# Kernel tuning notes

Hardware: AMD Instinct MI355X
Metric: run time of the kernel (lower is better)

The kernel has to match this reference:

```python
import jax, jax.numpy as jnp
import numpy as np

N0, N1, N2 = 120000, 40000, 10000   # sampled node counts per hop
E0, E1 = 600000, 150000             # edges per block (fanout ~15)
DIN, DH, NC = 128, 256, 47


def _glorot(k, fan_in, fan_out):
    s = (2.0 / (fan_in + fan_out)) ** 0.5
    return jax.random.normal(k, (fan_in, fan_out), jnp.float32) * s


def setup_inputs() -> dict:
    key = jax.random.key(0)
    ks = jax.random.split(key, 20)
    x0 = jax.random.normal(ks[0], (N0, DIN), jnp.float32)
    src0 = jax.random.randint(ks[1], (E0,), 0, N0)
    dst0 = jax.random.randint(ks[2], (E0,), 0, N1)
    src1 = jax.random.randint(ks[3], (E1,), 0, N1)
    dst1 = jax.random.randint(ks[4], (E1,), 0, N2)
    srcb0 = jax.random.randint(ks[5], (E0,), 0, N0)
    dstb0 = jax.random.randint(ks[6], (E0,), 0, N1)
    srcb1 = jax.random.randint(ks[7], (E1,), 0, N1)
    dstb1 = jax.random.randint(ks[8], (E1,), 0, N2)
    # id_old_value_new: must satisfy idx[:n] < n for every truncation length n,
    # i.e. idx[k] in [0, k+1)
    rng = np.random.default_rng(0)
    idx = jnp.asarray((rng.random(N0) * (np.arange(N0) + 1)).astype(np.int64))
    mix_ratio = jnp.float32(0.5)
    Wl0 = _glorot(ks[9], DIN, DH); Wr0 = _glorot(ks[10], DIN, DH)
    b0 = jnp.zeros((DH,), jnp.float32)
    Wl1 = _glorot(ks[11], DH, DH); Wr1 = _glorot(ks[12], DH, DH)
    b1 = jnp.zeros((DH,), jnp.float32)
    Wlin = _glorot(ks[13], DH, NC)
    blin = jnp.zeros((NC,), jnp.float32)
    return dict(x0=x0, src0=src0, dst0=dst0, src1=src1, dst1=dst1,
                srcb0=srcb0, dstb0=dstb0, srcb1=srcb1, dstb1=dstb1,
                idx=idx, mix_ratio=mix_ratio,
                Wl0=Wl0, Wr0=Wr0, b0=b0, Wl1=Wl1, Wr1=Wr1, b1=b1,
                Wlin=Wlin, blin=blin)


def _sage(x_all, root_x, src, dst, n_root, Wl, Wr, b):
    # PyG-style SAGEConv, mean aggregation: lin_l(mean_j x_j) + lin_r(root)
    msgs = x_all[src]                                        # [E, D] gather
    s = jax.ops.segment_sum(msgs, dst, num_segments=n_root)  # [n_root, D]
    cnt = jax.ops.segment_sum(jnp.ones_like(dst, dtype=x_all.dtype), dst,
                              num_segments=n_root)
    mean = s / jnp.maximum(cnt, 1.0)[:, None]
    return mean @ Wl + root_x @ Wr + b


def reference(x0, src0, dst0, src1, dst1, srcb0, dstb0, srcb1, dstb1,
              idx, mix_ratio, Wl0, Wr0, b0, Wl1, Wr1, b1, Wlin, blin):
    blocks = [(src0, dst0, N1), (src1, dst1, N2)]
    blocks_b = [(srcb0, dstb0, N1), (srcb1, dstb1, N2)]
    params = [(Wl0, Wr0, b0), (Wl1, Wr1, b1)]
    m = mix_ratio

    # first branch (dropout omitted: inference mode)
    aggr_xs = [x0]
    for i in range(2):
        src, dst, n_root = blocks[i]
        Wl, Wr, b = params[i]
        root_x = aggr_xs[-1][:n_root]
        x = jax.nn.relu(_sage(aggr_xs[-1], root_x, src, dst, n_root, Wl, Wr, b))
        aggr_xs.append(x)

    # permuted branch via id_old_value_new gather
    aggr_xs_b = [x[idx[: x.shape[0]]] for x in aggr_xs]

    x_mix = aggr_xs[0] * m + aggr_xs_b[0] * (1.0 - m)
    for i in range(2):
        src, dst, n_root = blocks[i]
        srcb, dstb, n_root_b = blocks_b[i]
        Wl, Wr, b = params[i]
        x_new = jax.nn.relu(_sage(aggr_xs[i], x_mix[:n_root], src, dst,
                                  n_root, Wl, Wr, b))
        x_new_b = jax.nn.relu(_sage(aggr_xs_b[i], x_mix[:n_root_b], srcb, dstb,
                                    n_root_b, Wl, Wr, b))
        x_mix = x_new * m + x_new_b * (1.0 - m)

    logits = x_mix @ Wlin + blin
    return jax.nn.log_softmax(logits, axis=-1)
```

## Files before the change

kernel.cpp:

```cpp
#include <hip/hip_runtime.h>
#include <math.h>

#define N1C 40000
#define N2C 10000
#define DIN 128
#define DH  256
#define NC  47

#define TOTCNT (2 * N1C + 2 * N2C)
#define CAP 64

typedef __attribute__((ext_vector_type(8))) short v8s;
typedef __attribute__((ext_vector_type(4))) float v4f;

__device__ __forceinline__ unsigned short f2bf(float f) {
    unsigned int u = __float_as_uint(f);
    u += 0x7FFF + ((u >> 16) & 1);
    return (unsigned short)(u >> 16);
}
__device__ __forceinline__ float bf2f(unsigned int h) {
    return __uint_as_float(h << 16);
}

__device__ __forceinline__ unsigned char f2e4m3(float f) {
    unsigned int u = __float_as_uint(f);
    unsigned char s = (unsigned char)((u >> 24) & 0x80);
    float a = __uint_as_float(u & 0x7FFFFFFF);
    if (a > 448.0f) a = 448.0f;
    if (a < 0.015625f) {
        int k = (int)rintf(a * 512.0f);
        return s | (unsigned char)k;
    }
    unsigned int bits = __float_as_uint(a);
    int et = (int)(bits >> 23) - 127 + 7;
    unsigned int m32 = bits & 0x7FFFFF;
    unsigned int m3 = m32 >> 20;
    unsigned int rest = m32 & 0xFFFFF;
    if (rest > 0x80000 || (rest == 0x80000 && (m3 & 1))) m3++;
    if (m3 == 8) { m3 = 0; et++; }
    if (et > 15 || (et == 15 && m3 == 7)) return s | 0x7E;
    return s | (unsigned char)((et << 3) | m3);
}

__device__ __forceinline__ void build_lut(float* lut, int t) {
    if (t < 256) {
        int e = (t >> 3) & 15, mm = t & 7;
        float d = (e == 0) ? (float)mm * (1.0f / 512.0f)
                           : (1.0f + (float)mm * 0.125f) * exp2f((float)(e - 7));
        if (t & 0x80) d = -d;
        lut[t] = d;
    }
}

__global__ __launch_bounds__(256) void front_fused(
        const int* __restrict__ src0, const int* __restrict__ dst0,
        const int* __restrict__ srcb0, const int* __restrict__ dstb0,
        const int* __restrict__ src1, const int* __restrict__ dst1,
        const int* __restrict__ srcb1, const int* __restrict__ dstb1,
        const int* __restrict__ perm, int* __restrict__ cur,
        int* __restrict__ bucket, int E0, int E1, int nbFill,
        const float* __restrict__ x0, unsigned short* __restrict__ x0h,
        unsigned char* __restrict__ x0f, long n8, int nbConv,
        const float* __restrict__ Wl0, const float* __restrict__ Wr0,
        const float* __restrict__ Wl1, const float* __restrict__ Wr1,
        unsigned short* __restrict__ Wt0l, unsigned short* __restrict__ Wt0r,
        unsigned short* __restrict__ Wt1l, unsigned short* __restrict__ Wt1r) {
    int b = blockIdx.x, t = threadIdx.x;
    if (b < nbFill) {
        int e = b * 256 + t;
        int tot = 2 * E0 + 2 * E1;
        if (e >= tot) return;
        int s, bin;
        if (e < E0) {
            s = src0[e];                  bin = dst0[e];
        } else if (e < 2 * E0) {
            int le = e - E0;
            s = perm[srcb0[le]];          bin = N1C + dstb0[le];
        } else if (e < 2 * E0 + E1) {
            int le = e - 2 * E0;
            s = src1[le];                 bin = 2 * N1C + dst1[le];
        } else {
            int le = e - 2 * E0 - E1;
            s = perm[srcb1[le]];          bin = 2 * N1C + N2C + dstb1[le];
        }
        int pos = atomicAdd(&cur[bin], 1);
        if (pos < CAP) bucket[(size_t)bin * CAP + pos] = s;
    } else if (b < nbFill + nbConv) {
        long i = (long)(b - nbFill) * 256 + t;
        if (i >= n8) return;
        const float4* p = (const float4*)(x0 + i * 8);
        float4 a = p[0], c = p[1];
        float f[8] = {a.x, a.y, a.z, a.w, c.x, c.y, c.z, c.w};
        v8s o;
        unsigned int q0 = 0, q1 = 0;
#pragma unroll
        for (int j = 0; j < 8; j++) {
            o[j] = (short)f2bf(f[j]);
            unsigned int e8 = f2e4m3(f[j]);
            if (j < 4) q0 |= e8 << (8 * j); else q1 |= e8 << (8 * (j - 4));
        }
        *(v8s*)(x0h + i * 8) = o;
        uint2 q = {q0, q1};
        *(uint2*)(x0f + i * 8) = q;
    } else {
        int id = (b - nbFill - nbConv) * 256 + t;
        const int S0 = DIN * DH;
        const int S1 = DH * DH;
        const float* W; unsigned short* Wt; int K, loc;
        if (id < S0)                   { W = Wl0; Wt = Wt0l; K = DIN; loc = id; }
        else if (id < 2 * S0)          { W = Wr0; Wt = Wt0r; K = DIN; loc = id - S0; }
        else if (id < 2 * S0 + S1)     { W = Wl1; Wt = Wt1l; K = DH;  loc = id - 2 * S0; }
        else if (id < 2 * S0 + 2 * S1) { W = Wr1; Wt = Wt1r; K = DH;  loc = id - 2 * S0 - S1; }
        else return;
        int n = loc / K, k = loc - n * K;
        Wt[(size_t)n * K + k] = f2bf(W[(size_t)k * DH + n]);
    }
}

__global__ __launch_bounds__(256) void gather_mean_128f(
        const unsigned char* __restrict__ xf, const int* __restrict__ bucket,
        const int* __restrict__ cur, unsigned short* __restrict__ mean0,
        unsigned short* __restrict__ meanb0) {
    __shared__ float lut[256];
    build_lut(lut, threadIdx.x);
    __syncthreads();
    const int half = N1C / 4;
    int b = blockIdx.x;
    int binbase; unsigned short* outp; int rb;
    if (b < half) { binbase = 0;   outp = mean0;  rb = b; }
    else          { binbase = N1C; outp = meanb0; rb = b - half; }
    int row = rb * 4 + (threadIdx.x >> 6);
    int lane = threadIdx.x & 63;
    int bin = binbase + row;
    int cnt = min(cur[bin], CAP);
    const int* cs = bucket + (size_t)bin * CAP;
    float a0 = 0.0f, a1 = 0.0f;
    int i = 0;
    for (; i + 3 < cnt; i += 4) {
        int s0 = cs[i], s1 = cs[i + 1], s2 = cs[i + 2], s3 = cs[i + 3];
        unsigned int u0 = *(const unsigned short*)&xf[(size_t)s0 * DIN + lane * 2];
        unsigned int u1 = *(const unsigned short*)&xf[(size_t)s1 * DIN + lane * 2];
        unsigned int u2 = *(const unsigned short*)&xf[(size_t)s2 * DIN + lane * 2];
        unsigned int u3 = *(const unsigned short*)&xf[(size_t)s3 * DIN + lane * 2];
        a0 += lut[u0 & 0xFF] + lut[u1 & 0xFF] + lut[u2 & 0xFF] + lut[u3 & 0xFF];
        a1 += lut[u0 >> 8] + lut[u1 >> 8] + lut[u2 >> 8] + lut[u3 >> 8];
    }
    for (; i < cnt; i++) {
        unsigned int u = *(const unsigned short*)&xf[(size_t)cs[i] * DIN + lane * 2];
        a0 += lut[u & 0xFF];
        a1 += lut[u >> 8];
    }
    float inv = 1.0f / (float)max(cnt, 1);
    unsigned int o = (unsigned int)f2bf(a0 * inv) | ((unsigned int)f2bf(a1 * inv) << 16);
    *(unsigned int*)&outp[(size_t)row * DIN + lane * 2] = o;
}

__global__ __launch_bounds__(256) void gather_mean_256f(
        const unsigned char* __restrict__ xf, const int* __restrict__ bucket,
        const int* __restrict__ cur, unsigned short* __restrict__ mean1,
        unsigned short* __restrict__ meanb1) {
    __shared__ float lut[256];
    build_lut(lut, threadIdx.x);
    __syncthreads();
    const int half = N2C / 4;
    int b = blockIdx.x;
    int binbase; unsigned short* outp; int rb;
    if (b < half) { binbase = 2 * N1C;       outp = mean1;  rb = b; }
    else          { binbase = 2 * N1C + N2C; outp = meanb1; rb = b - half; }
    int row = rb * 4 + (threadIdx.x >> 6);
    int lane = threadIdx.x & 63;
    int bin = binbase + row;
    int cnt = min(cur[bin], CAP);
    const int* cs = bucket + (size_t)bin * CAP;
    float a0 = 0.0f, a1 = 0.0f, a2 = 0.0f, a3 = 0.0f;
    int i = 0;
    for (; i + 1 < cnt; i += 2) {
        unsigned int u = *(const unsigned int*)&xf[(size_t)cs[i] * DH + lane * 4];
        unsigned int v = *(const unsigned int*)&xf[(size_t)cs[i + 1] * DH + lane * 4];
        a0 += lut[u & 0xFF] + lut[v & 0xFF];
        a1 += lut[(u >> 8) & 0xFF] + lut[(v >> 8) & 0xFF];
        a2 += lut[(u >> 16) & 0xFF] + lut[(v >> 16) & 0xFF];
        a3 += lut[u >> 24] + lut[v >> 24];
    }
    if (i < cnt) {
        unsigned int u = *(const unsigned int*)&xf[(size_t)cs[i] * DH + lane * 4];
        a0 += lut[u & 0xFF]; a1 += lut[(u >> 8) & 0xFF];
        a2 += lut[(u >> 16) & 0xFF]; a3 += lut[u >> 24];
    }
    float inv = 1.0f / (float)max(cnt, 1);
    uint2 o;
    o.x = (unsigned int)f2bf(a0 * inv) | ((unsigned int)f2bf(a1 * inv) << 16);
    o.y = (unsigned int)f2bf(a2 * inv) | ((unsigned int)f2bf(a3 * inv) << 16);
    *(uint2*)&outp[(size_t)row * DH + lane * 4] = o;
}

#define KP0 136
#define H0T 5
__global__ __launch_bounds__(256, 2) void hop0_mfma(
        const unsigned short* __restrict__ x0h, const int* __restrict__ idx,
        const unsigned short* __restrict__ mean0, const unsigned short* __restrict__ meanb0,
        const unsigned short* __restrict__ Wtl, const unsigned short* __restrict__ Wtr,
        const float* __restrict__ b, const float* __restrict__ mixp,
        unsigned char* __restrict__ x1f, unsigned short* __restrict__ xm1) {
    __shared__ unsigned short Alds[4][16][KP0];
    int t = threadIdx.x;
    int wv = t >> 6, lane = t & 63;
    int mrow = lane & 15, quad = lane >> 4;
    float m = *mixp;

    v8s wl[4][4], wr[4][4];
    float bb[4];
#pragma unroll
    for (int ct = 0; ct < 4; ct++) {
        int n = wv * 64 + ct * 16 + mrow;
        bb[ct] = b[n];
#pragma unroll
        for (int ks = 0; ks < 4; ks++) {
            int k0 = ks * 32 + quad * 8;
            wl[ct][ks] = *(const v8s*)&Wtl[(size_t)n * DIN + k0];
            wr[ct][ks] = *(const v8s*)&Wtr[(size_t)n * DIN + k0];
        }
    }

    for (int tile = 0; tile < H0T; tile++) {
        int row0 = (blockIdx.x * H0T + tile) * 16;
        {
            int r = t >> 4, k0 = (t & 15) * 8;
            int rg = row0 + r;
            *(v8s*)&Alds[0][r][k0] = *(const v8s*)&mean0[(size_t)rg * DIN + k0];
            *(v8s*)&Alds[1][r][k0] = *(const v8s*)&meanb0[(size_t)rg * DIN + k0];
            v8s xr = *(const v8s*)&x0h[(size_t)rg * DIN + k0];
            int ib = idx[rg];
            v8s xb = *(const v8s*)&x0h[(size_t)ib * DIN + k0];
            v8s vm;
#pragma unroll
            for (int j = 0; j < 8; j++) {
                float fr = bf2f((unsigned short)xr[j]);
                float fb = bf2f((unsigned short)xb[j]);
                vm[j] = (short)f2bf(m * fr + (1.0f - m) * fb);
            }
            *(v8s*)&Alds[2][r][k0] = xr;
            *(v8s*)&Alds[3][r][k0] = vm;
        }
        __syncthreads();
        v4f accA[4], accB[4], accC[4], accD[4];
#pragma unroll
        for (int ct = 0; ct < 4; ct++) {
            accA[ct] = (v4f){0.f, 0.f, 0.f, 0.f}; accB[ct] = (v4f){0.f, 0.f, 0.f, 0.f};
            accC[ct] = (v4f){0.f, 0.f, 0.f, 0.f}; accD[ct] = (v4f){0.f, 0.f, 0.f, 0.f};
        }
#pragma unroll
        for (int ks = 0; ks < 4; ks++) {
            int k0 = ks * 32 + quad * 8;
            v8s aM = *(v8s*)&Alds[0][mrow][k0];
            v8s aB = *(v8s*)&Alds[1][mrow][k0];
            v8s aR = *(v8s*)&Alds[2][mrow][k0];
            v8s aX = *(v8s*)&Alds[3][mrow][k0];
#pragma unroll
            for (int ct = 0; ct < 4; ct++) {
                accA[ct] = __builtin_amdgcn_mfma_f32_16x16x32_bf16(aM, wl[ct][ks], accA[ct], 0, 0, 0);
                accB[ct] = __builtin_amdgcn_mfma_f32_16x16x32_bf16(aB, wl[ct][ks], accB[ct], 0, 0, 0);
                accC[ct] = __builtin_amdgcn_mfma_f32_16x16x32_bf16(aR, wr[ct][ks], accC[ct], 0, 0, 0);
                accD[ct] = __builtin_amdgcn_mfma_f32_16x16x32_bf16(aX, wr[ct][ks], accD[ct], 0, 0, 0);
            }
        }
#pragma unroll
        for (int ct = 0; ct < 4; ct++) {
            int col = wv * 64 + ct * 16 + mrow;
#pragma unroll
            for (int r = 0; r < 4; r++) {
                int row = row0 + quad * 4 + r;
                float pA = accA[ct][r], pB = accB[ct][r], pC = accC[ct][r], pD = accD[ct][r];
                float xv  = fmaxf(pA + pC + bb[ct], 0.0f);
                float xn  = fmaxf(pA + pD + bb[ct], 0.0f);
                float xnb = fmaxf(pB + pD + bb[ct], 0.0f);
                x1f[(size_t)row * DH + col] = f2e4m3(xv);
                xm1[(size_t)row * DH + col] = f2bf(m * xn + (1.0f - m) * xnb);
            }
        }
        __syncthreads();
    }
}

#define KP1 264
#define H1T 2
__global__ __launch_bounds__(256, 2) void hop1_mfma(
        const unsigned short* __restrict__ mean1, const unsigned short* __restrict__ meanb1,
        const unsigned short* __restrict__ xm1,
        const unsigned short* __restrict__ Wtl, const unsigned short* __restrict__ Wtr,
        const float* __restrict__ b, const float* __restrict__ mixp,
        float* __restrict__ xm2) {
    __shared__ unsigned short Alds[3][16][KP1];
    int t = threadIdx.x;
    int wv = t >> 6, lane = t & 63;
    int mrow = lane & 15, quad = lane >> 4;
    float m = *mixp;

    v8s wlc[4][4], wrc[4][4];
    float bb[4];
#pragma unroll
    for (int ct = 0; ct < 4; ct++) {
        int n = wv * 64 + ct * 16 + mrow;
        bb[ct] = b[n];
#pragma unroll
        for (int ks = 0; ks < 4; ks++) {
            int k0 = ks * 32 + quad * 8;
            wlc[ct][ks] = *(const v8s*)&Wtl[(size_t)n * DH + k0];
            wrc[ct][ks] = *(const v8s*)&Wtr[(size_t)n * DH + k0];
        }
    }

    for (int tt = 0; tt < H1T; tt++) {
        int tIdx = blockIdx.x * H1T + tt;
        if (tIdx >= N2C / 16) break;
        int row0 = tIdx * 16;
        {
            int r = t >> 4, k0 = (t & 15) * 16;
            int rg = row0 + r;
            *(v8s*)&Alds[0][r][k0]     = *(const v8s*)&mean1[(size_t)rg * DH + k0];
            *(v8s*)&Alds[0][r][k0 + 8] = *(const v8s*)&mean1[(size_t)rg * DH + k0 + 8];
            *(v8s*)&Alds[1][r][k0]     = *(const v8s*)&meanb1[(size_t)rg * DH + k0];
            *(v8s*)&Alds[1][r][k0 + 8] = *(const v8s*)&meanb1[(size_t)rg * DH + k0 + 8];
            *(v8s*)&Alds[2][r][k0]     = *(const v8s*)&xm1[(size_t)rg * DH + k0];
            *(v8s*)&Alds[2][r][k0 + 8] = *(const v8s*)&xm1[(size_t)rg * DH + k0 + 8];
        }
        __syncthreads();
        v4f accA[4], accB[4], accC[4];
#pragma unroll
        for (int ct = 0; ct < 4; ct++) {
            accA[ct] = (v4f){0.f, 0.f, 0.f, 0.f};
            accB[ct] = (v4f){0.f, 0.f, 0.f, 0.f};
            accC[ct] = (v4f){0.f, 0.f, 0.f, 0.f};
        }
#pragma unroll
        for (int ks = 0; ks < 8; ks++) {
            int k0 = ks * 32 + quad * 8;
            v8s aM = *(v8s*)&Alds[0][mrow][k0];
            v8s aB = *(v8s*)&Alds[1][mrow][k0];
            v8s aR = *(v8s*)&Alds[2][mrow][k0];
#pragma unroll
            for (int ct = 0; ct < 4; ct++) {
                v8s bl, br;
                if (ks < 4) { bl = wlc[ct][ks]; br = wrc[ct][ks]; }
                else {
                    int n = wv * 64 + ct * 16 + mrow;
                    bl = *(const v8s*)&Wtl[(size_t)n * DH + k0];
                    br = *(const v8s*)&Wtr[(size_t)n * DH + k0];
                }
                accA[ct] = __builtin_amdgcn_mfma_f32_16x16x32_bf16(aM, bl, accA[ct], 0, 0, 0);
                accB[ct] = __builtin_amdgcn_mfma_f32_16x16x32_bf16(aB, bl, accB[ct], 0, 0, 0);
                accC[ct] = __builtin_amdgcn_mfma_f32_16x16x32_bf16(aR, br, accC[ct], 0, 0, 0);
            }
        }
#pragma unroll
        for (int ct = 0; ct < 4; ct++) {
            int col = wv * 64 + ct * 16 + mrow;
#pragma unroll
            for (int r = 0; r < 4; r++) {
                int row = row0 + quad * 4 + r;
                float xn  = fmaxf(accA[ct][r] + accC[ct][r] + bb[ct], 0.0f);
                float xnb = fmaxf(accB[ct][r] + accC[ct][r] + bb[ct], 0.0f);
                xm2[(size_t)row * DH + col] = m * xn + (1.0f - m) * xnb;
            }
        }
        __syncthreads();
    }
}

__global__ __launch_bounds__(256) void logits_lsm(
        const float* __restrict__ xmix2, const float* __restrict__ Wlin,
        const float* __restrict__ blin, float* __restrict__ out, int nrows) {
    int w = threadIdx.x >> 6;
    int row = blockIdx.x * 4 + w;
    if (row >= nrows) return;
    int t = threadIdx.x & 63;
    __shared__ float xs[4][DH];
    for (int i = t; i < DH; i += 64) xs[w][i] = xmix2[(size_t)row * DH + i];
    __builtin_amdgcn_s_waitcnt(0);
    float acc = 0.0f;
    if (t < NC) {
        acc = blin[t];
        for (int k = 0; k < DH; k++) acc += xs[w][k] * Wlin[k * NC + t];
    }
    float v = (t < NC) ? acc : -INFINITY;
    float mx = v;
    for (int off = 32; off; off >>= 1) mx = fmaxf(mx, __shfl_xor(mx, off, 64));
    float ex = (t < NC) ? expf(acc - mx) : 0.0f;
    float sum = ex;
    for (int off = 32; off; off >>= 1) sum += __shfl_xor(sum, off, 64);
    if (t < NC) out[(size_t)row * NC + t] = acc - mx - logf(sum);
}

extern "C" void kernel_launch(void* const* d_in, const int* in_sizes, int n_in,
                              void* d_out, int out_size, void* d_ws, size_t ws_size,
                              hipStream_t stream) {
    const float* x0    = (const float*)d_in[0];
    const int*   src0  = (const int*)d_in[1];
    const int*   dst0  = (const int*)d_in[2];
    const int*   src1  = (const int*)d_in[3];
    const int*   dst1  = (const int*)d_in[4];
    const int*   srcb0 = (const int*)d_in[5];
    const int*   dstb0 = (const int*)d_in[6];
    const int*   srcb1 = (const int*)d_in[7];
    const int*   dstb1 = (const int*)d_in[8];
    const int*   idx   = (const int*)d_in[9];
    const float* mixp  = (const float*)d_in[10];
    const float* Wl0   = (const float*)d_in[11];
    const float* Wr0   = (const float*)d_in[12];
    const float* b0    = (const float*)d_in[13];
    const float* Wl1   = (const float*)d_in[14];
    const float* Wr1   = (const float*)d_in[15];
    const float* b1    = (const float*)d_in[16];
    const float* Wlin  = (const float*)d_in[17];
    const float* blin  = (const float*)d_in[18];
    float* out = (float*)d_out;

    const int E0 = in_sizes[1];
    const int E1 = in_sizes[3];
    const long x0elems = (long)in_sizes[0];

    int* wsi    = (int*)d_ws;
    int* cur    = wsi;
    int* bucket = cur + TOTCNT;
    unsigned short* wsh = (unsigned short*)(bucket + (size_t)TOTCNT * CAP);
    unsigned short* mean0  = wsh;
    unsigned short* meanb0 = mean0  + (size_t)N1C * DIN;
    unsigned short* mean1  = meanb0 + (size_t)N1C * DIN;
    unsigned short* meanb1 = mean1  + (size_t)N2C * DH;
    unsigned short* xm1h   = meanb1 + (size_t)N2C * DH;
    unsigned short* x0h    = xm1h   + (size_t)N1C * DH;
    unsigned short* Wt0l   = x0h    + (size_t)x0elems;
    unsigned short* Wt0r   = Wt0l + DIN * DH;
    unsigned short* Wt1l   = Wt0r + DIN * DH;
    unsigned short* Wt1r   = Wt1l + DH * DH;
    unsigned char* x0f = (unsigned char*)(Wt1r + DH * DH);
    unsigned char* x1f = x0f + (size_t)x0elems;
    float* xm2 = (float*)(x1f + (size_t)N1C * DH + 8);

    hipMemsetAsync(cur, 0, sizeof(int) * TOTCNT, stream);

    int etot = 2 * E0 + 2 * E1;
    int nbFill = (etot + 255) / 256;
    long n8 = x0elems / 8;
    int nbConv = (int)((n8 + 255) / 256);
    int nbW = (2 * DIN * DH + 2 * DH * DH + 255) / 256;
    front_fused<<<nbFill + nbConv + nbW, 256, 0, stream>>>(
        src0, dst0, srcb0, dstb0, src1, dst1, srcb1, dstb1, idx, cur, bucket,
        E0, E1, nbFill, x0, x0h, x0f, n8, nbConv,
        Wl0, Wr0, Wl1, Wr1, Wt0l, Wt0r, Wt1l, Wt1r);

    gather_mean_128f<<<2 * (N1C / 4), 256, 0, stream>>>(x0f, bucket, cur, mean0, meanb0);

    hop0_mfma<<<N1C / (16 * H0T), 256, 0, stream>>>(x0h, idx, mean0, meanb0, Wt0l, Wt0r,
                                                    b0, mixp, x1f, xm1h);

    gather_mean_256f<<<2 * (N2C / 4), 256, 0, stream>>>(x1f, bucket, cur, mean1, meanb1);

    hop1_mfma<<<(N2C / 16 + H1T - 1) / H1T, 256, 0, stream>>>(mean1, meanb1, xm1h,
                                                              Wt1l, Wt1r, b1, mixp, xm2);

    logits_lsm<<<(N2C + 3) / 4, 256, 0, stream>>>(xm2, Wlin, blin, out, N2C);
}
```

Before: 383.6 us.

## Use hardware FP8 decode, widen 128-dim gather, drop bf16 copy of x0

Replaces the shared-memory LUT FP8 decode with the packed fp8-to-f32 conversion builtin when the compiler provides it. The 128-wide gather now has each lane load 4 bytes, so one wavefront covers two rows and the block count is halved. The bf16 copy of x0 is no longer written in the front kernel; hop0 reads the fp32 x0 directly and converts to bf16 itself. This removes a full bf16 write of x0 and its later re-read, but hop0 now loads twice as many bytes for the root and permuted rows, and the hardware path depends on the builtin's FP8 format matching the software e4m3 encoding.

Result: faster. 366.3 us (-4.5%).

```diff
diff --git a/kernel.cpp b/kernel.cpp
--- a/kernel.cpp
+++ b/kernel.cpp
@@ -12,6 +12,11 @@
 
 typedef __attribute__((ext_vector_type(8))) short v8s;
 typedef __attribute__((ext_vector_type(4))) float v4f;
+typedef __attribute__((ext_vector_type(2))) float v2f;
+
+#if __has_builtin(__builtin_amdgcn_cvt_pk_f32_fp8)
+#define HW_FP8 1
+#endif
 
 __device__ __forceinline__ unsigned short f2bf(float f) {
     unsigned int u = __float_as_uint(f);
@@ -42,6 +47,7 @@
     return s | (unsigned char)((et << 3) | m3);
 }
 
+#ifndef HW_FP8
 __device__ __forceinline__ void build_lut(float* lut, int t) {
     if (t < 256) {
         int e = (t >> 3) & 15, mm = t & 7;
@@ -51,6 +57,19 @@
         lut[t] = d;
     }
 }
+#endif
+
+__device__ __forceinline__ void dec4(unsigned int u, float& f0, float& f1,
+                                     float& f2, float& f3, const float* lut) {
+#ifdef HW_FP8
+    v2f lo = __builtin_amdgcn_cvt_pk_f32_fp8((int)u, false);
+    v2f hi = __builtin_amdgcn_cvt_pk_f32_fp8((int)u, true);
+    f0 = lo[0]; f1 = lo[1]; f2 = hi[0]; f3 = hi[1];
+#else
+    f0 = lut[u & 0xFF]; f1 = lut[(u >> 8) & 0xFF];
+    f2 = lut[(u >> 16) & 0xFF]; f3 = lut[u >> 24];
+#endif
+}
 
 __global__ __launch_bounds__(256) void front_fused(
         const int* __restrict__ src0, const int* __restrict__ dst0,
@@ -59,8 +78,8 @@
         const int* __restrict__ srcb1, const int* __restrict__ dstb1,
         const int* __restrict__ perm, int* __restrict__ cur,
         int* __restrict__ bucket, int E0, int E1, int nbFill,
-        const float* __restrict__ x0, unsigned short* __restrict__ x0h,
-        unsigned char* __restrict__ x0f, long n8, int nbConv,
+        const float* __restrict__ x0, unsigned char* __restrict__ x0f,
+        long n8, int nbConv,
         const float* __restrict__ Wl0, const float* __restrict__ Wr0,
         const float* __restrict__ Wl1, const float* __restrict__ Wr1,
         unsigned short* __restrict__ Wt0l, unsigned short* __restrict__ Wt0r,
@@ -91,15 +110,12 @@
         const float4* p = (const float4*)(x0 + i * 8);
         float4 a = p[0], c = p[1];
         float f[8] = {a.x, a.y, a.z, a.w, c.x, c.y, c.z, c.w};
-        v8s o;
         unsigned int q0 = 0, q1 = 0;
 #pragma unroll
         for (int j = 0; j < 8; j++) {
-            o[j] = (short)f2bf(f[j]);
             unsigned int e8 = f2e4m3(f[j]);
             if (j < 4) q0 |= e8 << (8 * j); else q1 |= e8 << (8 * (j - 4));
         }
-        *(v8s*)(x0h + i * 8) = o;
         uint2 q = {q0, q1};
         *(uint2*)(x0f + i * 8) = q;
     } else {
@@ -121,47 +137,61 @@
         const unsigned char* __restrict__ xf, const int* __restrict__ bucket,
         const int* __restrict__ cur, unsigned short* __restrict__ mean0,
         unsigned short* __restrict__ meanb0) {
-    __shared__ float lut[256];
-    build_lut(lut, threadIdx.x);
+#ifndef HW_FP8
+    __shared__ float lutm[256];
+    build_lut(lutm, threadIdx.x);
     __syncthreads();
-    const int half = N1C / 4;
+    const float* lut = lutm;
+#else
+    const float* lut = nullptr;
+#endif
+    const int half = N1C / 8;
     int b = blockIdx.x;
     int binbase; unsigned short* outp; int rb;
     if (b < half) { binbase = 0;   outp = mean0;  rb = b; }
     else          { binbase = N1C; outp = meanb0; rb = b - half; }
-    int row = rb * 4 + (threadIdx.x >> 6);
-    int lane = threadIdx.x & 63;
+    int wv = threadIdx.x >> 6, lane = threadIdx.x & 63;
+    int row = rb * 8 + wv * 2 + (lane >> 5);
+    int c4 = (lane & 31) * 4;
     int bin = binbase + row;
     int cnt = min(cur[bin], CAP);
     const int* cs = bucket + (size_t)bin * CAP;
-    float a0 = 0.0f, a1 = 0.0f;
+    float a0 = 0.0f, a1 = 0.0f, a2 = 0.0f, a3 = 0.0f;
     int i = 0;
-    for (; i + 3 < cnt; i += 4) {
-        int s0 = cs[i], s1 = cs[i + 1], s2 = cs[i + 2], s3 = cs[i + 3];
-        unsigned int u0 = *(const unsigned short*)&xf[(size_t)s0 * DIN + lane * 2];
-        unsigned int u1 = *(const unsigned short*)&xf[(size_t)s1 * DIN + lane * 2];
-        unsigned int u2 = *(const unsigned short*)&xf[(size_t)s2 * DIN + lane * 2];
-        unsigned int u3 = *(const unsigned short*)&xf[(size_t)s3 * DIN + lane * 2];
-        a0 += lut[u0 & 0xFF] + lut[u1 & 0xFF] + lut[u2 & 0xFF] + lut[u3 & 0xFF];
-        a1 += lut[u0 >> 8] + lut[u1 >> 8] + lut[u2 >> 8] + lut[u3 >> 8];
-    }
-    for (; i < cnt; i++) {
-        unsigned int u = *(const unsigned short*)&xf[(size_t)cs[i] * DIN + lane * 2];
-        a0 += lut[u & 0xFF];
-        a1 += lut[u >> 8];
+    for (; i + 1 < cnt; i += 2) {
+        int s0 = cs[i], s1 = cs[i + 1];
+        unsigned int u = *(const unsigned int*)&xf[(size_t)s0 * DIN + c4];
+        unsigned int v = *(const unsigned int*)&xf[(size_t)s1 * DIN + c4];
+        float u0, u1, u2, u3, w0, w1, w2, w3;
+        dec4(u, u0, u1, u2, u3, lut);
+        dec4(v, w0, w1, w2, w3, lut);
+        a0 += u0 + w0; a1 += u1 + w1; a2 += u2 + w2; a3 += u3 + w3;
+    }
+    if (i < cnt) {
+        unsigned int u = *(const unsigned int*)&xf[(size_t)cs[i] * DIN + c4];
+        float u0, u1, u2, u3;
+        dec4(u, u0, u1, u2, u3, lut);
+        a0 += u0; a1 += u1; a2 += u2; a3 += u3;
     }
     float inv = 1.0f / (float)max(cnt, 1);
-    unsigned int o = (unsigned int)f2bf(a0 * inv) | ((unsigned int)f2bf(a1 * inv) << 16);
-    *(unsigned int*)&outp[(size_t)row * DIN + lane * 2] = o;
+    uint2 o;
+    o.x = (unsigned int)f2bf(a0 * inv) | ((unsigned int)f2bf(a1 * inv) << 16);
+    o.y = (unsigned int)f2bf(a2 * inv) | ((unsigned int)f2bf(a3 * inv) << 16);
+    *(uint2*)&outp[(size_t)row * DIN + c4] = o;
 }
 
 __global__ __launch_bounds__(256) void gather_mean_256f(
         const unsigned char* __restrict__ xf, const int* __restrict__ bucket,
         const int* __restrict__ cur, unsigned short* __restrict__ mean1,
         unsigned short* __restrict__ meanb1) {
-    __shared__ float lut[256];
-    build_lut(lut, threadIdx.x);
+#ifndef HW_FP8
+    __shared__ float lutm[256];
+    build_lut(lutm, threadIdx.x);
     __syncthreads();
+    const float* lut = lutm;
+#else
+    const float* lut = nullptr;
+#endif
     const int half = N2C / 4;
     int b = blockIdx.x;
     int binbase; unsigned short* outp; int rb;
@@ -175,17 +205,19 @@
     float a0 = 0.0f, a1 = 0.0f, a2 = 0.0f, a3 = 0.0f;
     int i = 0;
     for (; i + 1 < cnt; i += 2) {
-        unsigned int u = *(const unsigned int*)&xf[(size_t)cs[i] * DH + lane * 4];
-        unsigned int v = *(const unsigned int*)&xf[(size_t)cs[i + 1] * DH + lane * 4];
-        a0 += lut[u & 0xFF] + lut[v & 0xFF];
-        a1 += lut[(u >> 8) & 0xFF] + lut[(v >> 8) & 0xFF];
-        a2 += lut[(u >> 16) & 0xFF] + lut[(v >> 16) & 0xFF];
-        a3 += lut[u >> 24] + lut[v >> 24];
+        int s0 = cs[i], s1 = cs[i + 1];
+        unsigned int u = *(const unsigned int*)&xf[(size_t)s0 * DH + lane * 4];
+        unsigned int v = *(const unsigned int*)&xf[(size_t)s1 * DH + lane * 4];
+        float u0, u1, u2, u3, w0, w1, w2, w3;
+        dec4(u, u0, u1, u2, u3, lut);
+        dec4(v, w0, w1, w2, w3, lut);
+        a0 += u0 + w0; a1 += u1 + w1; a2 += u2 + w2; a3 += u3 + w3;
     }
     if (i < cnt) {
         unsigned int u = *(const unsigned int*)&xf[(size_t)cs[i] * DH + lane * 4];
-        a0 += lut[u & 0xFF]; a1 += lut[(u >> 8) & 0xFF];
-        a2 += lut[(u >> 16) & 0xFF]; a3 += lut[u >> 24];
+        float u0, u1, u2, u3;
+        dec4(u, u0, u1, u2, u3, lut);
+        a0 += u0; a1 += u1; a2 += u2; a3 += u3;
     }
     float inv = 1.0f / (float)max(cnt, 1);
     uint2 o;
@@ -197,7 +229,7 @@
 #define KP0 136
 #define H0T 5
 __global__ __launch_bounds__(256, 2) void hop0_mfma(
-        const unsigned short* __restrict__ x0h, const int* __restrict__ idx,
+        const float* __restrict__ x0, const int* __restrict__ idx,
         const unsigned short* __restrict__ mean0, const unsigned short* __restrict__ meanb0,
         const unsigned short* __restrict__ Wtl, const unsigned short* __restrict__ Wtr,
         const float* __restrict__ b, const float* __restrict__ mixp,
@@ -229,17 +261,20 @@
             int rg = row0 + r;
             *(v8s*)&Alds[0][r][k0] = *(const v8s*)&mean0[(size_t)rg * DIN + k0];
             *(v8s*)&Alds[1][r][k0] = *(const v8s*)&meanb0[(size_t)rg * DIN + k0];
-            v8s xr = *(const v8s*)&x0h[(size_t)rg * DIN + k0];
+            const float4* xr4 = (const float4*)&x0[(size_t)rg * DIN + k0];
+            float4 A0 = xr4[0], A1 = xr4[1];
             int ib = idx[rg];
-            v8s xb = *(const v8s*)&x0h[(size_t)ib * DIN + k0];
-            v8s vm;
+            const float4* xb4 = (const float4*)&x0[(size_t)ib * DIN + k0];
+            float4 B0 = xb4[0], B1 = xb4[1];
+            float fa[8] = {A0.x, A0.y, A0.z, A0.w, A1.x, A1.y, A1.z, A1.w};
+            float fb[8] = {B0.x, B0.y, B0.z, B0.w, B1.x, B1.y, B1.z, B1.w};
+            v8s vr, vm;
 #pragma unroll
             for (int j = 0; j < 8; j++) {
-                float fr = bf2f((unsigned short)xr[j]);
-                float fb = bf2f((unsigned short)xb[j]);
-                vm[j] = (short)f2bf(m * fr + (1.0f - m) * fb);
+                vr[j] = (short)f2bf(fa[j]);
+                vm[j] = (short)f2bf(m * fa[j] + (1.0f - m) * fb[j]);
             }
-            *(v8s*)&Alds[2][r][k0] = xr;
+            *(v8s*)&Alds[2][r][k0] = vr;
             *(v8s*)&Alds[3][r][k0] = vm;
         }
         __syncthreads();
@@ -428,14 +463,13 @@
     unsigned short* mean1  = meanb0 + (size_t)N1C * DIN;
     unsigned short* meanb1 = mean1  + (size_t)N2C * DH;
     unsigned short* xm1h   = meanb1 + (size_t)N2C * DH;
-    unsigned short* x0h    = xm1h   + (size_t)N1C * DH;
-    unsigned short* Wt0l   = x0h    + (size_t)x0elems;
+    unsigned short* Wt0l   = xm1h   + (size_t)N1C * DH;
     unsigned short* Wt0r   = Wt0l + DIN * DH;
     unsigned short* Wt1l   = Wt0r + DIN * DH;
     unsigned short* Wt1r   = Wt1l + DH * DH;
-    unsigned char* x0f = (unsigned char*)(Wt1r + DH * DH);
+    float* xm2 = (float*)(Wt1r + DH * DH);
+    unsigned char* x0f = (unsigned char*)(xm2 + (size_t)N2C * DH);
     unsigned char* x1f = x0f + (size_t)x0elems;
-    float* xm2 = (float*)(x1f + (size_t)N1C * DH + 8);
 
     hipMemsetAsync(cur, 0, sizeof(int) * TOTCNT, stream);
 
@@ -446,12 +480,12 @@
     int nbW = (2 * DIN * DH + 2 * DH * DH + 255) / 256;
     front_fused<<<nbFill + nbConv + nbW, 256, 0, stream>>>(
         src0, dst0, srcb0, dstb0, src1, dst1, srcb1, dstb1, idx, cur, bucket,
-        E0, E1, nbFill, x0, x0h, x0f, n8, nbConv,
+        E0, E1, nbFill, x0, x0f, n8, nbConv,
         Wl0, Wr0, Wl1, Wr1, Wt0l, Wt0r, Wt1l, Wt1r);
 
-    gather_mean_128f<<<2 * (N1C / 4), 256, 0, stream>>>(x0f, bucket, cur, mean0, meanb0);
-
-    hop0_mfma<<<N1C / (16 * H0T), 256, 0, stream>>>(x0h, idx, mean0, meanb0, Wt0l, Wt0r,
+    gather_mean_128f<<<2 * (N1C / 8), 256, 0, stream>>>(x0f, bucket, cur, mean0, meanb0);
+
+    hop0_mfma<<<N1C / (16 * H0T), 256, 0, stream>>>(x0, idx, mean0, meanb0, Wt0l, Wt0r,
                                                     b0, mixp, x1f, xm1h);
 
     gather_mean_256f<<<2 * (N2C / 4), 256, 0, stream>>>(x1f, bucket, cur, mean1, meanb1);
```
